# Optimization experiments

Measured on AMD Instinct MI355X. Metric: run time of the kernel, lower is better.

The kernel has to match this reference:

```python
import jax, jax.numpy as jnp
import numpy as np

T, N, M = 16, 10000, 2048          # timesteps, total nodes, masked nodes per step
F_IN, F1, F2, H = 256, 256, 256, 256  # feats_per_node, layer_1, layer_2, lstm_feats


def setup_inputs() -> dict:
    key = jax.random.key(0)
    ks = jax.random.split(key, 9)
    A = jax.random.normal(ks[0], (T, M, M), jnp.float32) / np.float32(np.sqrt(M))
    node_feats = jax.random.normal(ks[1], (N, F_IN), jnp.float32)
    # unique sorted indices per timestep (scatter target must be duplicate-free)
    mask = jax.vmap(lambda k: jnp.sort(jax.random.permutation(k, N)[:M]))(
        jax.random.split(ks[2], T)).astype(jnp.int32)
    u = lambda k, sh, fan: jax.random.uniform(k, sh, jnp.float32, -1.0, 1.0) * (2.0 / np.sqrt(fan))
    w0 = u(ks[3], (F_IN, F1), F_IN)
    w1 = u(ks[4], (F1, F2), F1)
    s = 1.0 / np.sqrt(H)
    W_ih = jax.random.uniform(ks[5], (4 * H, F2), jnp.float32, -s, s)
    W_hh = jax.random.uniform(ks[6], (4 * H, H), jnp.float32, -s, s)
    b_ih = jax.random.uniform(ks[7], (4 * H,), jnp.float32, -s, s)
    b_hh = jax.random.uniform(ks[8], (4 * H,), jnp.float32, -s, s)
    return {"A": A, "node_feats": node_feats, "mask": mask, "w0": w0, "w1": w1,
            "W_ih": W_ih, "W_hh": W_hh, "b_ih": b_ih, "b_hh": b_hh}


def reference(A, node_feats, mask, w0, w1, W_ih, W_hh, b_ih, b_hh):
    def gcn_step(Ah, idx):
        # layer 0: x = X @ W0 ; x[idx] = act(Ahat @ x[idx])
        x = node_feats @ w0                               # [N, F1]
        x = x.at[idx].set(jax.nn.relu(Ah @ x[idx]))
        # layer 1
        x = x @ w1                                        # [N, F2]
        x = x.at[idx].set(jax.nn.relu(Ah @ x[idx]))
        return x

    seq = jax.vmap(gcn_step)(A, mask)                     # [T, N, F2]

    def lstm_step(carry, xt):
        h, c = carry
        z = xt @ W_ih.T + h @ W_hh.T + (b_ih + b_hh)      # [N, 4H]
        i, f, g, o = jnp.split(z, 4, axis=-1)             # torch gate order i,f,g,o
        c = jax.nn.sigmoid(f) * c + jax.nn.sigmoid(i) * jnp.tanh(g)
        h = jax.nn.sigmoid(o) * jnp.tanh(c)
        return (h, c), None

    h0 = jnp.zeros((N, H), seq.dtype)
    (h, _), _ = jax.lax.scan(lstm_step, (h0, h0), seq)
    return h                                              # out[-1] of single-layer LSTM
```

## Files before the change

kernel.cpp:

```cpp
#include <hip/hip_runtime.h>
#include <cstdint>
#include <cstddef>

#pragma clang diagnostic ignored "-Waddress-space-conversion"

constexpr int T  = 16;
constexpr int N  = 10000;
constexpr int M  = 2048;
constexpr int F  = 256;
constexpr int H  = 256;
constexpr int G4 = 1024;
constexpr int NP = 10112;

typedef _Float16 f16;
using half8  = __attribute__((ext_vector_type(8))) f16;
using half4  = __attribute__((ext_vector_type(4))) f16;
using half2v = __attribute__((ext_vector_type(2))) f16;
using f32x4  = __attribute__((ext_vector_type(4))) float;

typedef __attribute__((address_space(1))) const void gas_t;
typedef __attribute__((address_space(3))) void las_t;

__device__ __forceinline__ void gl_lds16(const f16* g, f16* l) {
    __builtin_amdgcn_global_load_lds((gas_t*)g, (las_t*)l, 16, 0, 0);
}

template<bool AF32, bool RELU, int OMODE>
__global__ __launch_bounds__(256, 2)
void gemm16(const void* __restrict__ Ag, long long sA,
            const f16*  __restrict__ Bg, long long sB,
            void*       __restrict__ Cg, long long sC,
            int Kk, int Nn, int Mvalid, int ldct)
{
    __shared__ f16 Als[2][128 * 32];
    __shared__ f16 Bls[2][128 * 32];

    const int tid  = threadIdx.x;
    const int lane = tid & 63;
    const int w    = tid >> 6;
    const int wm   = w >> 1, wn = w & 1;
    const int m0   = blockIdx.y * 128, n0 = blockIdx.x * 128;
    const int z    = blockIdx.z;

    const f16* Bt = Bg + (size_t)z * sB;
    const int srow = lane >> 2;
    const int scol = (lane & 3) * 8;

    f32x4 acc[4][4] = {};

    auto stage = [&](int buf, int kt) {
        const int k0 = kt * 32;
        #pragma unroll
        for (int c = 0; c < 2; ++c) {
            const int brow = w * 32 + c * 16;
            gl_lds16(Bt + (size_t)(n0 + brow + srow) * Kk + k0 + scol,
                     &Bls[buf][brow * 32]);
        }
        if constexpr (AF32) {
            const float* Af = (const float*)Ag + (size_t)z * sA;
            #pragma unroll
            for (int p = 0; p < 4; ++p) {
                const int flat = p * 1024 + tid * 4;
                const int r = flat >> 5, cc = flat & 31;
                float4 v = *(const float4*)&Af[(size_t)(m0 + r) * Kk + k0 + cc];
                half4 hv = { (f16)v.x, (f16)v.y, (f16)v.z, (f16)v.w };
                *(half4*)&Als[buf][r * 32 + cc] = hv;
            }
        } else {
            const f16* Af = (const f16*)Ag + (size_t)z * sA;
            #pragma unroll
            for (int c = 0; c < 2; ++c) {
                const int arow = w * 32 + c * 16;
                gl_lds16(Af + (size_t)(m0 + arow + srow) * Kk + k0 + scol,
                         &Als[buf][arow * 32]);
            }
        }
    };

    const int nk = Kk >> 5;
    stage(0, 0);
    int cur = 0;
    const int fr = lane & 15, fg = lane >> 4;

    for (int kt = 0; kt < nk; ++kt) {
        __syncthreads();
        if (kt + 1 < nk) stage(cur ^ 1, kt + 1);

        half8 a[4], b[4];
        #pragma unroll
        for (int i = 0; i < 4; ++i)
            a[i] = *(const half8*)&Als[cur][(wm * 64 + i * 16 + fr) * 32 + fg * 8];
        #pragma unroll
        for (int j = 0; j < 4; ++j)
            b[j] = *(const half8*)&Bls[cur][(wn * 64 + j * 16 + fr) * 32 + fg * 8];
        #pragma unroll
        for (int i = 0; i < 4; ++i)
            #pragma unroll
            for (int j = 0; j < 4; ++j)
                acc[i][j] = __builtin_amdgcn_mfma_f32_16x16x32_f16(a[i], b[j], acc[i][j], 0, 0, 0);
        cur ^= 1;
    }

    #pragma unroll
    for (int i = 0; i < 4; ++i) {
        const int gmb = m0 + wm * 64 + i * 16 + fg * 4;
        #pragma unroll
        for (int j = 0; j < 4; ++j) {
            const int gn = n0 + wn * 64 + j * 16 + fr;
            f32x4 v = acc[i][j];
            if (RELU) {
                v[0] = fmaxf(v[0], 0.f); v[1] = fmaxf(v[1], 0.f);
                v[2] = fmaxf(v[2], 0.f); v[3] = fmaxf(v[3], 0.f);
            }
            if constexpr (OMODE == 1) {
                f16* Ch = (f16*)Cg + (size_t)z * sC;
                #pragma unroll
                for (int r = 0; r < 4; ++r)
                    if (gmb + r < Mvalid) Ch[(size_t)(gmb + r) * Nn + gn] = (f16)v[r];
            } else {
                f16* Ct = (f16*)Cg + (size_t)z * sC;
                half4 hv = { (f16)v[0], (f16)v[1], (f16)v[2], (f16)v[3] };
                if (gmb + 3 < Mvalid) *(half4*)&Ct[(size_t)gn * ldct + gmb] = hv;
            }
        }
    }
}

__global__ __launch_bounds__(256, 2)
void gemm_lstm(const f16* __restrict__ h16, const f16* __restrict__ Whh,
               const f16* __restrict__ U, const f16* __restrict__ V,
               const int* __restrict__ invt, const float* __restrict__ bsum,
               float* __restrict__ Cb, f16* __restrict__ h16_out,
               float* __restrict__ hout)
{
    __shared__ f16 Als[2][128 * 32];
    __shared__ f16 Bls[2][128 * 32];

    const int tid  = threadIdx.x;
    const int lane = tid & 63;
    const int w    = tid >> 6;
    const int wm   = w >> 1, wn = w & 1;
    const int m0   = blockIdx.y * 128, n0 = blockIdx.x * 128;

    const int srow = lane >> 2;
    const int scol = (lane & 3) * 8;

    f32x4 acc[4][4] = {};

    auto stage = [&](int buf, int kt) {
        const int k0 = kt * 32;
        #pragma unroll
        for (int c = 0; c < 2; ++c) {
            const int row = w * 32 + c * 16;
            gl_lds16(Whh + (size_t)(n0 + row + srow) * H + k0 + scol, &Bls[buf][row * 32]);
            gl_lds16(h16 + (size_t)(m0 + row + srow) * H + k0 + scol, &Als[buf][row * 32]);
        }
    };

    stage(0, 0);
    int cur = 0;
    const int fr = lane & 15, fg = lane >> 4;

    for (int kt = 0; kt < H / 32; ++kt) {
        __syncthreads();
        if (kt + 1 < H / 32) stage(cur ^ 1, kt + 1);
        half8 a[4], b[4];
        #pragma unroll
        for (int i = 0; i < 4; ++i)
            a[i] = *(const half8*)&Als[cur][(wm * 64 + i * 16 + fr) * 32 + fg * 8];
        #pragma unroll
        for (int j = 0; j < 4; ++j)
            b[j] = *(const half8*)&Bls[cur][(wn * 64 + j * 16 + fr) * 32 + fg * 8];
        #pragma unroll
        for (int i = 0; i < 4; ++i)
            #pragma unroll
            for (int j = 0; j < 4; ++j)
                acc[i][j] = __builtin_amdgcn_mfma_f32_16x16x32_f16(a[i], b[j], acc[i][j], 0, 0, 0);
        cur ^= 1;
    }

    const int u = ((n0 >> 6) + wn) * 16 + fr;
    const int colbase = n0 + wn * 64 + fr;
    const float b0 = bsum[colbase], b1 = bsum[colbase + 16],
                b2 = bsum[colbase + 32], b3 = bsum[colbase + 48];
    auto sig = [](float x) { return 1.f / (1.f + __expf(-x)); };

    #pragma unroll
    for (int i = 0; i < 4; ++i) {
        const int nodeb = m0 + wm * 64 + i * 16 + fg * 4;
        #pragma unroll
        for (int r = 0; r < 4; ++r) {
            const int node = nodeb + r;
            if (node >= N) continue;
            const int p = invt[node];
            const f16* xb = (p >= 0) ? V + (size_t)p * G4 : U + (size_t)node * G4;
            const float zi = acc[i][0][r] + (float)xb[colbase]      + b0;
            const float zf = acc[i][1][r] + (float)xb[colbase + 16] + b1;
            const float zg = acc[i][2][r] + (float)xb[colbase + 32] + b2;
            const float zo = acc[i][3][r] + (float)xb[colbase + 48] + b3;
            const size_t ci = (size_t)node * H + u;
            const float c = sig(zf) * Cb[ci] + sig(zi) * tanhf(zg);
            Cb[ci] = c;
            const float hv = sig(zo) * tanhf(c);
            h16_out[ci] = (f16)hv;
            if (hout) hout[ci] = hv;
        }
    }
}

__global__ __launch_bounds__(256)
void gather_T(const f16* __restrict__ Y0h, const int* __restrict__ mask,
              f16* __restrict__ GT)
{
    __shared__ f16 tile[64][F + 8];
    const int t = blockIdx.y, p0 = blockIdx.x * 64;
    const int tid = threadIdx.x;
    const int pr = tid >> 2;
    const int fc = (tid & 3) * 8;

    const int row = mask[t * M + p0 + pr];
    const f16* src = Y0h + (size_t)row * F;
    #pragma unroll
    for (int it = 0; it < 8; ++it) {
        const int f = it * 32 + fc;
        *(half8*)&tile[pr][f] = *(const half8*)&src[f];
    }
    __syncthreads();

    f16* dst = GT + ((size_t)t * F + tid) * M + p0;
    #pragma unroll
    for (int pc = 0; pc < 64; pc += 8) {
        half8 v;
        #pragma unroll
        for (int r = 0; r < 8; ++r) v[r] = tile[pc + r][tid];
        *(half8*)&dst[pc] = v;
    }
}

__global__ void cvt_f16(const float* __restrict__ s, f16* __restrict__ d, long long n)
{
    long long base = ((long long)blockIdx.x * blockDim.x + threadIdx.x) * 4;
    if (base + 3 < n) {
        float4 v = *(const float4*)&s[base];
        half4 hv = { (f16)v.x, (f16)v.y, (f16)v.z, (f16)v.w };
        *(half4*)&d[base] = hv;
    } else {
        for (long long k = base; k < n; ++k) d[k] = (f16)s[k];
    }
}

__global__ void cvtT_f16(const float* __restrict__ s, f16* __restrict__ d, int R, int C)
{
    int i = blockIdx.x * 256 + threadIdx.x;
    if (i >= R * C) return;
    int r = i % R, c = i / R;
    d[(size_t)c * R + r] = (f16)s[(size_t)r * C + c];
}

__global__ void permW(const float* __restrict__ s, f16* __restrict__ d, int K)
{
    const int pcol = blockIdx.x;
    const int c64 = pcol >> 6, within = pcol & 63, gate = within >> 4, r = within & 15;
    const int srow = gate * 256 + c64 * 16 + r;
    const float* sp = s + (size_t)srow * K;
    f16* dp = d + (size_t)pcol * K;
    const int k = threadIdx.x * 4;
    float4 v = *(const float4*)&sp[k];
    half4 hv = { (f16)v.x, (f16)v.y, (f16)v.z, (f16)v.w };
    *(half4*)&dp[k] = hv;
}

__global__ void bias_perm(const float* __restrict__ bi, const float* __restrict__ bh,
                          float* __restrict__ bsum)
{
    const int pcol = blockIdx.x * 256 + threadIdx.x;
    if (pcol >= G4) return;
    const int c64 = pcol >> 6, within = pcol & 63, gate = within >> 4, r = within & 15;
    const int srow = gate * 256 + c64 * 16 + r;
    bsum[pcol] = bi[srow] + bh[srow];
}

__global__ void build_inv(const int* __restrict__ mask, int* __restrict__ inv)
{
    int i = blockIdx.x * blockDim.x + threadIdx.x;
    if (i >= T * M) return;
    int t = i / M;
    inv[(size_t)t * N + mask[i]] = i % M;
}

extern "C" void kernel_launch(void* const* d_in, const int* in_sizes, int n_in,
                              void* d_out, int out_size, void* d_ws, size_t ws_size,
                              hipStream_t stream)
{
    const float* A_all = (const float*)d_in[0];
    const float* nf    = (const float*)d_in[1];
    const int*   mask  = (const int*)  d_in[2];
    const float* w0    = (const float*)d_in[3];
    const float* w1    = (const float*)d_in[4];
    const float* W_ih  = (const float*)d_in[5];
    const float* W_hh  = (const float*)d_in[6];
    const float* b_ih  = (const float*)d_in[7];
    const float* b_hh  = (const float*)d_in[8];
    float* h = (float*)d_out;

    char* wp = (char*)d_ws;
    auto alloc = [&](size_t bytes) { char* p = wp; wp += (bytes + 255) & ~(size_t)255; return p; };
    f16*   nf16  = (f16*)alloc((size_t)NP * F * 2);
    f16*   w0T   = (f16*)alloc((size_t)F * F * 2);
    f16*   w1T   = (f16*)alloc((size_t)F * F * 2);
    f16*   Wih16 = (f16*)alloc((size_t)G4 * F * 2);
    f16*   Whh16 = (f16*)alloc((size_t)G4 * H * 2);
    float* bsum  = (float*)alloc((size_t)G4 * 4);
    f16*   Y0h   = (f16*)alloc((size_t)NP * F * 2);
    f16*   Y1h   = (f16*)alloc((size_t)NP * F * 2);
    f16*   Uh    = (f16*)alloc((size_t)NP * G4 * 2);
    f16*   GT    = (f16*)alloc((size_t)T * F * M * 2);
    f16*   Z1b   = (f16*)alloc((size_t)T * M * F * 2);
    f16*   Z2T   = (f16*)alloc((size_t)T * F * M * 2);
    f16*   Z3b   = (f16*)alloc((size_t)T * M * F * 2);
    f16*   Vb    = (f16*)alloc((size_t)4 * M * G4 * 2);
    float* Cb    = (float*)alloc((size_t)N * H * 4);
    f16*   h16   = (f16*)alloc((size_t)NP * H * 2);
    int*   inv   = (int*)alloc((size_t)T * N * 4);

    hipMemsetAsync(Cb,  0,    (size_t)N * H * 4,  stream);
    hipMemsetAsync(h16, 0,    (size_t)NP * H * 2, stream);
    hipMemsetAsync(nf16,0,    (size_t)NP * F * 2, stream);
    hipMemsetAsync(inv, 0xFF, (size_t)T * N * 4,  stream);

    build_inv<<<(T * M + 255) / 256, 256, 0, stream>>>(mask, inv);
    cvt_f16 <<<((long long)N * F / 4 + 255) / 256, 256, 0, stream>>>(nf, nf16, (long long)N * F);
    cvtT_f16<<<(F * F + 255) / 256, 256, 0, stream>>>(w0, w0T, F, F);
    cvtT_f16<<<(F * F + 255) / 256, 256, 0, stream>>>(w1, w1T, F, F);
    permW<<<G4, 64, 0, stream>>>(W_ih, Wih16, F);
    permW<<<G4, 64, 0, stream>>>(W_hh, Whh16, H);
    bias_perm<<<(G4 + 255) / 256, 256, 0, stream>>>(b_ih, b_hh, bsum);

    gemm16<false,false,1><<<dim3(F / 128,  NP / 128, 1), 256, 0, stream>>>(nf16, 0, w0T,   0, Y0h, 0, F, F,  NP, 0);
    gemm16<false,false,1><<<dim3(F / 128,  NP / 128, 1), 256, 0, stream>>>(Y0h,  0, w1T,   0, Y1h, 0, F, F,  NP, 0);
    gemm16<false,false,1><<<dim3(G4 / 128, NP / 128, 1), 256, 0, stream>>>(Y1h,  0, Wih16, 0, Uh,  0, F, G4, NP, 0);

    gather_T<<<dim3(M / 64, T), 256, 0, stream>>>(Y0h, mask, GT);

    const long long sAmm = (long long)M * M;
    const long long sFM  = (long long)F * M;
    const long long sMF  = (long long)M * F;
    gemm16<true, true, 1><<<dim3(2, 16, T), 256, 0, stream>>>(A_all, sAmm, GT,  sFM, Z1b, sMF, M, F, M, 0);
    gemm16<false,false,2><<<dim3(2, 16, T), 256, 0, stream>>>(Z1b,  sMF,  w1T, 0,   Z2T, sFM, F, F, M, M);
    gemm16<true, true, 1><<<dim3(2, 16, T), 256, 0, stream>>>(A_all, sAmm, Z2T, sFM, Z3b, sMF, M, F, M, 0);

    for (int t = 0; t < T; ++t) {
        if ((t & 3) == 0) {
            gemm16<false,false,1><<<dim3(G4 / 128, M / 128, 4), 256, 0, stream>>>(
                Z3b + (size_t)t * M * F, sMF, Wih16, 0, Vb, (long long)M * G4, F, G4, M, 0);
        }
        gemm_lstm<<<dim3(G4 / 128, NP / 128, 1), 256, 0, stream>>>(
            h16, Whh16, Uh, Vb + (size_t)(t & 3) * M * G4, inv + (size_t)t * N,
            bsum, Cb, h16, (t == T - 1) ? h : nullptr);
    }
}
```

Baseline: 792.7 us.

## Fold bias into input GEMMs, store LSTM cell in fp16, batch V projection

Bias is now added in the epilogue of the U and V input-projection GEMMs, which removes the per-element bias loads from the LSTM step kernel. The LSTM cell state is stored as fp16 instead of fp32 to halve its read/write traffic, at some cost in accuracy. The V projection runs as a single launch over all timesteps instead of once every four steps, which needs a larger buffer. The A-GEMMs are also split into chunks of 8 timesteps with swapped grid axes, and occupancy hints rise from 2 to 3 blocks per CU.

```diff
diff --git a/kernel.cpp b/kernel.cpp
--- a/kernel.cpp
+++ b/kernel.cpp
@@ -15,7 +15,6 @@
 typedef _Float16 f16;
 using half8  = __attribute__((ext_vector_type(8))) f16;
 using half4  = __attribute__((ext_vector_type(4))) f16;
-using half2v = __attribute__((ext_vector_type(2))) f16;
 using f32x4  = __attribute__((ext_vector_type(4))) float;
 
 typedef __attribute__((address_space(1))) const void gas_t;
@@ -25,12 +24,13 @@
     __builtin_amdgcn_global_load_lds((gas_t*)g, (las_t*)l, 16, 0, 0);
 }
 
-template<bool AF32, bool RELU, int OMODE>
-__global__ __launch_bounds__(256, 2)
+template<bool AF32, bool RELU, int OMODE, bool SWAP>
+__global__ __launch_bounds__(256, 3)
 void gemm16(const void* __restrict__ Ag, long long sA,
             const f16*  __restrict__ Bg, long long sB,
             void*       __restrict__ Cg, long long sC,
-            int Kk, int Nn, int Mvalid, int ldct)
+            int Kk, int Nn, int Mvalid, int ldct,
+            const float* __restrict__ bias)
 {
     __shared__ f16 Als[2][128 * 32];
     __shared__ f16 Bls[2][128 * 32];
@@ -39,7 +39,8 @@
     const int lane = tid & 63;
     const int w    = tid >> 6;
     const int wm   = w >> 1, wn = w & 1;
-    const int m0   = blockIdx.y * 128, n0 = blockIdx.x * 128;
+    const int m0   = (SWAP ? blockIdx.x : blockIdx.y) * 128;
+    const int n0   = (SWAP ? blockIdx.y : blockIdx.x) * 128;
     const int z    = blockIdx.z;
 
     const f16* Bt = Bg + (size_t)z * sB;
@@ -102,15 +103,17 @@
     }
 
     #pragma unroll
-    for (int i = 0; i < 4; ++i) {
-        const int gmb = m0 + wm * 64 + i * 16 + fg * 4;
-        #pragma unroll
-        for (int j = 0; j < 4; ++j) {
-            const int gn = n0 + wn * 64 + j * 16 + fr;
+    for (int j = 0; j < 4; ++j) {
+        const int gn = n0 + wn * 64 + j * 16 + fr;
+        const float bb = bias ? bias[gn] : 0.f;
+        #pragma unroll
+        for (int i = 0; i < 4; ++i) {
+            const int gmb = m0 + wm * 64 + i * 16 + fg * 4;
             f32x4 v = acc[i][j];
-            if (RELU) {
-                v[0] = fmaxf(v[0], 0.f); v[1] = fmaxf(v[1], 0.f);
-                v[2] = fmaxf(v[2], 0.f); v[3] = fmaxf(v[3], 0.f);
+            #pragma unroll
+            for (int r = 0; r < 4; ++r) {
+                v[r] += bb;
+                if (RELU) v[r] = fmaxf(v[r], 0.f);
             }
             if constexpr (OMODE == 1) {
                 f16* Ch = (f16*)Cg + (size_t)z * sC;
@@ -126,11 +129,11 @@
     }
 }
 
-__global__ __launch_bounds__(256, 2)
+__global__ __launch_bounds__(256, 3)
 void gemm_lstm(const f16* __restrict__ h16, const f16* __restrict__ Whh,
                const f16* __restrict__ U, const f16* __restrict__ V,
-               const int* __restrict__ invt, const float* __restrict__ bsum,
-               float* __restrict__ Cb, f16* __restrict__ h16_out,
+               const int* __restrict__ invt,
+               f16* __restrict__ Cb, f16* __restrict__ h16_out,
                float* __restrict__ hout)
 {
     __shared__ f16 Als[2][128 * 32];
@@ -181,8 +184,6 @@
 
     const int u = ((n0 >> 6) + wn) * 16 + fr;
     const int colbase = n0 + wn * 64 + fr;
-    const float b0 = bsum[colbase], b1 = bsum[colbase + 16],
-                b2 = bsum[colbase + 32], b3 = bsum[colbase + 48];
     auto sig = [](float x) { return 1.f / (1.f + __expf(-x)); };
 
     #pragma unroll
@@ -194,13 +195,13 @@
             if (node >= N) continue;
             const int p = invt[node];
             const f16* xb = (p >= 0) ? V + (size_t)p * G4 : U + (size_t)node * G4;
-            const float zi = acc[i][0][r] + (float)xb[colbase]      + b0;
-            const float zf = acc[i][1][r] + (float)xb[colbase + 16] + b1;
-            const float zg = acc[i][2][r] + (float)xb[colbase + 32] + b2;
-            const float zo = acc[i][3][r] + (float)xb[colbase + 48] + b3;
+            const float zi = acc[i][0][r] + (float)xb[colbase];
+            const float zf = acc[i][1][r] + (float)xb[colbase + 16];
+            const float zg = acc[i][2][r] + (float)xb[colbase + 32];
+            const float zo = acc[i][3][r] + (float)xb[colbase + 48];
             const size_t ci = (size_t)node * H + u;
-            const float c = sig(zf) * Cb[ci] + sig(zi) * tanhf(zg);
-            Cb[ci] = c;
+            const float c = sig(zf) * (float)Cb[ci] + sig(zi) * tanhf(zg);
+            Cb[ci] = (f16)c;
             const float hv = sig(zo) * tanhf(c);
             h16_out[ci] = (f16)hv;
             if (hout) hout[ci] = hv;
@@ -318,12 +319,12 @@
     f16*   Z1b   = (f16*)alloc((size_t)T * M * F * 2);
     f16*   Z2T   = (f16*)alloc((size_t)T * F * M * 2);
     f16*   Z3b   = (f16*)alloc((size_t)T * M * F * 2);
-    f16*   Vb    = (f16*)alloc((size_t)4 * M * G4 * 2);
-    float* Cb    = (float*)alloc((size_t)N * H * 4);
+    f16*   Vb    = (f16*)alloc((size_t)T * M * G4 * 2);
+    f16*   Cb    = (f16*)alloc((size_t)N * H * 2);
     f16*   h16   = (f16*)alloc((size_t)NP * H * 2);
     int*   inv   = (int*)alloc((size_t)T * N * 4);
 
-    hipMemsetAsync(Cb,  0,    (size_t)N * H * 4,  stream);
+    hipMemsetAsync(Cb,  0,    (size_t)N * H * 2,  stream);
     hipMemsetAsync(h16, 0,    (size_t)NP * H * 2, stream);
     hipMemsetAsync(nf16,0,    (size_t)NP * F * 2, stream);
     hipMemsetAsync(inv, 0xFF, (size_t)T * N * 4,  stream);
@@ -336,26 +337,35 @@
     permW<<<G4, 64, 0, stream>>>(W_hh, Whh16, H);
     bias_perm<<<(G4 + 255) / 256, 256, 0, stream>>>(b_ih, b_hh, bsum);
 
-    gemm16<false,false,1><<<dim3(F / 128,  NP / 128, 1), 256, 0, stream>>>(nf16, 0, w0T,   0, Y0h, 0, F, F,  NP, 0);
-    gemm16<false,false,1><<<dim3(F / 128,  NP / 128, 1), 256, 0, stream>>>(Y0h,  0, w1T,   0, Y1h, 0, F, F,  NP, 0);
-    gemm16<false,false,1><<<dim3(G4 / 128, NP / 128, 1), 256, 0, stream>>>(Y1h,  0, Wih16, 0, Uh,  0, F, G4, NP, 0);
+    gemm16<false,false,1,false><<<dim3(F / 128,  NP / 128, 1), 256, 0, stream>>>(nf16, 0, w0T,   0, Y0h, 0, F, F,  NP, 0, nullptr);
+    gemm16<false,false,1,false><<<dim3(F / 128,  NP / 128, 1), 256, 0, stream>>>(Y0h,  0, w1T,   0, Y1h, 0, F, F,  NP, 0, nullptr);
+    gemm16<false,false,1,false><<<dim3(G4 / 128, NP / 128, 1), 256, 0, stream>>>(Y1h,  0, Wih16, 0, Uh,  0, F, G4, NP, 0, bsum);
 
     gather_T<<<dim3(M / 64, T), 256, 0, stream>>>(Y0h, mask, GT);
 
     const long long sAmm = (long long)M * M;
     const long long sFM  = (long long)F * M;
     const long long sMF  = (long long)M * F;
-    gemm16<true, true, 1><<<dim3(2, 16, T), 256, 0, stream>>>(A_all, sAmm, GT,  sFM, Z1b, sMF, M, F, M, 0);
-    gemm16<false,false,2><<<dim3(2, 16, T), 256, 0, stream>>>(Z1b,  sMF,  w1T, 0,   Z2T, sFM, F, F, M, M);
-    gemm16<true, true, 1><<<dim3(2, 16, T), 256, 0, stream>>>(A_all, sAmm, Z2T, sFM, Z3b, sMF, M, F, M, 0);
+
+    constexpr int CH = 8;
+    for (int c0 = 0; c0 < T; c0 += CH) {
+        gemm16<true, true, 1,true ><<<dim3(16, 2, CH), 256, 0, stream>>>(
+            (const char*)A_all + (size_t)c0 * sAmm * 4, sAmm,
+            GT + (size_t)c0 * sFM, sFM, Z1b + (size_t)c0 * sMF, sMF, M, F, M, 0, nullptr);
+        gemm16<false,false,2,false><<<dim3(2, 16, CH), 256, 0, stream>>>(
+            Z1b + (size_t)c0 * sMF, sMF, w1T, 0,
+            Z2T + (size_t)c0 * sFM, sFM, F, F, M, M, nullptr);
+        gemm16<true, true, 1,true ><<<dim3(16, 2, CH), 256, 0, stream>>>(
+            (const char*)A_all + (size_t)c0 * sAmm * 4, sAmm,
+            Z2T + (size_t)c0 * sFM, sFM, Z3b + (size_t)c0 * sMF, sMF, M, F, M, 0, nullptr);
+    }
+
+    gemm16<false,false,1,false><<<dim3(G4 / 128, M / 128, T), 256, 0, stream>>>(
+        Z3b, sMF, Wih16, 0, Vb, (long long)M * G4, F, G4, M, 0, bsum);
 
     for (int t = 0; t < T; ++t) {
-        if ((t & 3) == 0) {
-            gemm16<false,false,1><<<dim3(G4 / 128, M / 128, 4), 256, 0, stream>>>(
-                Z3b + (size_t)t * M * F, sMF, Wih16, 0, Vb, (long long)M * G4, F, G4, M, 0);
-        }
         gemm_lstm<<<dim3(G4 / 128, NP / 128, 1), 256, 0, stream>>>(
-            h16, Whh16, Uh, Vb + (size_t)(t & 3) * M * G4, inv + (size_t)t * N,
-            bsum, Cb, h16, (t == T - 1) ? h : nullptr);
-    }
-}
+            h16, Whh16, Uh, Vb + (size_t)t * M * G4, inv + (size_t)t * N,
+            Cb, h16, (t == T - 1) ? h : nullptr);
+    }
+}
```

New measurement: 955.9 us. +20.6%, slower.
